# Performance work log

Hardware: AMD Instinct MI355X
Metric: run time of the kernel (lower is better)

The kernel has to match this reference:

```python
import jax, jax.numpy as jnp
import numpy as np

B, L, E, H = 1, 4096, 1024, 16
D = E // H
EPS = 1e-6


def setup_inputs() -> dict:
    key = jax.random.key(0)
    k1, k2, k3 = jax.random.split(key, 3)
    # fan-in scaled init to keep activations sane
    x = jax.random.normal(k1, (B, L, E), dtype=jnp.float32)
    qkv_w = jax.random.normal(k2, (E, 3 * E), dtype=jnp.float32) / np.sqrt(E)
    qkv_b = jnp.zeros((3 * E,), dtype=jnp.float32)
    out_w = jax.random.normal(k3, (E, E), dtype=jnp.float32) / np.sqrt(E)
    out_b = jnp.zeros((E,), dtype=jnp.float32)
    return {"x": x, "qkv_w": qkv_w, "qkv_b": qkv_b, "out_w": out_w, "out_b": out_b}


def reference(x, qkv_w, qkv_b, out_w, out_b):
    b, l, e = x.shape
    qkv = x @ qkv_w + qkv_b                      # (B, L, 3E)
    q, k, v = jnp.split(qkv, 3, axis=-1)
    # (B, L, E) -> (B, H, L, D)
    q = q.reshape(b, l, H, D).transpose(0, 2, 1, 3)
    k = k.reshape(b, l, H, D).transpose(0, 2, 1, 3)
    v = v.reshape(b, l, H, D).transpose(0, 2, 1, 3)
    q_prime = jax.nn.elu(q) + 1.0
    k_prime = jax.nn.elu(k) + 1.0
    # cumulative sum of per-position outer products k'_l v_l^T : (B,H,L,D,D)
    kv_prod = jnp.einsum('bhld,bhle->bhlde', k_prime, v)
    kv_cumsum = jnp.cumsum(kv_prod, axis=2)
    context = jnp.einsum('bhld,bhlde->bhle', q_prime, kv_cumsum)  # (B,H,L,D)
    k_cumsum = jnp.cumsum(k_prime, axis=2)                        # (B,H,L,D)
    norm = jnp.einsum('bhld,bhld->bhl', q_prime, k_cumsum)        # (B,H,L)
    output = context / (norm[..., None] + EPS)
    output = output.transpose(0, 2, 1, 3).reshape(b, l, e)
    return output @ out_w + out_b
```

## Files before the change

kernel.cpp:

```cpp
#include <hip/hip_runtime.h>
#include <cstddef>
#include <cstdint>

#define L_SEQ 4096
#define EMB   1024
#define NH    16
#define HD    64
#define N3    3072
#define CHUNK 64
#define NCHUNK 64
#define EPS 1e-6f

typedef __attribute__((ext_vector_type(8))) short   bf16x8;
typedef __attribute__((ext_vector_type(4))) short   bf16x4;
typedef __attribute__((ext_vector_type(4))) float   floatx4;

#define AS1 __attribute__((address_space(1)))
#define AS3 __attribute__((address_space(3)))

__device__ __forceinline__ void gload_lds16(const void* g, void* l) {
    __builtin_amdgcn_global_load_lds((AS1 const unsigned int*)g,
                                     (AS3 unsigned int*)l, 16, 0, 0);
}

__device__ __forceinline__ short f2bf(float f) {
    union { float f; unsigned u; } a; a.f = f;
    unsigned r = a.u + 0x7fffu + ((a.u >> 16) & 1u);
    return (short)(r >> 16);
}
__device__ __forceinline__ float bf2f(short s) {
    union { unsigned u; float f; } a; a.u = ((unsigned)(unsigned short)s) << 16;
    return a.f;
}

__global__ __launch_bounds__(256)
void convert_bf16(const float* __restrict__ in, short* __restrict__ out, int n8)
{
    const int i = blockIdx.x * 256 + threadIdx.x;
    if (i < n8) {
        const floatx4 a = *(const floatx4*)(in + (size_t)i * 8);
        const floatx4 b = *(const floatx4*)(in + (size_t)i * 8 + 4);
        bf16x8 o;
        o[0] = f2bf(a[0]); o[1] = f2bf(a[1]); o[2] = f2bf(a[2]); o[3] = f2bf(a[3]);
        o[4] = f2bf(b[0]); o[5] = f2bf(b[1]); o[6] = f2bf(b[2]); o[7] = f2bf(b[3]);
        *(bf16x8*)(out + (size_t)i * 8) = o;
    }
}

__global__ __launch_bounds__(256)
void transpose_bf16(const float* __restrict__ W, short* __restrict__ WT,
                    int K, int N)
{
    __shared__ float t[64][65];
    const int bx = blockIdx.x, by = blockIdx.y;
    const int tid = threadIdx.x;
    const int r  = tid >> 4;
    const int c4 = (tid & 15) << 2;
#pragma unroll
    for (int s = 0; s < 4; ++s) {
        const int k = r + s * 16;
        const floatx4 v = *(const floatx4*)&W[(size_t)(by * 64 + k) * N + bx * 64 + c4];
        t[k][c4 + 0] = v[0]; t[k][c4 + 1] = v[1];
        t[k][c4 + 2] = v[2]; t[k][c4 + 3] = v[3];
    }
    __syncthreads();
#pragma unroll
    for (int s = 0; s < 4; ++s) {
        const int n = r + s * 16;
        bf16x4 o;
        o[0] = f2bf(t[c4 + 0][n]); o[1] = f2bf(t[c4 + 1][n]);
        o[2] = f2bf(t[c4 + 2][n]); o[3] = f2bf(t[c4 + 3][n]);
        *(bf16x4*)&WT[(size_t)(bx * 64 + n) * K + by * 64 + c4] = o;
    }
}

template<int MODE>
__global__ __launch_bounds__(256)
void mfma_gemm(const short* __restrict__ A, const short* __restrict__ BT,
               const float* __restrict__ bias,
               short* __restrict__ OQ, short* __restrict__ OK, short* __restrict__ OV,
               float* __restrict__ OF, int N, int K)
{
    __shared__ short Asm[128 * 32];
    __shared__ short Bsm[128 * 32];
    const int tid  = threadIdx.x;
    const int lane = tid & 63;
    const int wave = tid >> 6;
    const int wm = (wave >> 1) * 64;
    const int wn = (wave & 1) * 64;
    const int bx = blockIdx.x;
    const int by = blockIdx.y;
    const int frow = lane & 15;
    const int fko  = (lane >> 4) << 3;

    const short* Ab = A  + (size_t)(by * 128) * K;
    const short* Bb = BT + (size_t)(bx * 128) * K;

    floatx4 acc[4][4] = {};

    for (int k0 = 0; k0 < K; k0 += 32) {
#pragma unroll
        for (int q = 0; q < 2; ++q) {
            const int ia = q * 256 + tid;
            const int row = ia >> 2;
            const int kc  = (ia & 3) << 3;
            gload_lds16(Ab + (size_t)row * K + k0 + kc, &Asm[ia << 3]);
            gload_lds16(Bb + (size_t)row * K + k0 + kc, &Bsm[ia << 3]);
        }
        __syncthreads();
        bf16x8 af[4], bfv[4];
#pragma unroll
        for (int mi = 0; mi < 4; ++mi)
            af[mi] = *(const bf16x8*)&Asm[(wm + mi * 16 + frow) * 32 + fko];
#pragma unroll
        for (int ni = 0; ni < 4; ++ni)
            bfv[ni] = *(const bf16x8*)&Bsm[(wn + ni * 16 + frow) * 32 + fko];
#pragma unroll
        for (int mi = 0; mi < 4; ++mi)
#pragma unroll
            for (int ni = 0; ni < 4; ++ni)
                acc[mi][ni] = __builtin_amdgcn_mfma_f32_16x16x32_bf16(
                    af[mi], bfv[ni], acc[mi][ni], 0, 0, 0);
        __syncthreads();
    }

    const int rq = (lane >> 4) << 2;
#pragma unroll
    for (int ni = 0; ni < 4; ++ni) {
        const int n = bx * 128 + wn + ni * 16 + frow;
        const float bv = bias[n];
        if (MODE == 0) {
            const int rsel = n >> 10;
            const int nn = n & 1023;
            const int h  = nn >> 6;
            const int d  = nn & 63;
            short* base = (rsel == 0) ? OQ : (rsel == 1 ? OK : OV);
            const bool do_elu = (rsel < 2);
#pragma unroll
            for (int mi = 0; mi < 4; ++mi) {
#pragma unroll
                for (int r = 0; r < 4; ++r) {
                    const int m = by * 128 + wm + mi * 16 + rq + r;
                    float v = acc[mi][ni][r] + bv;
                    if (do_elu) v = (v > 0.f) ? (v + 1.f) : expf(v);
                    base[((size_t)(h * L_SEQ + m)) * HD + d] = f2bf(v);
                }
            }
        } else {
#pragma unroll
            for (int mi = 0; mi < 4; ++mi) {
#pragma unroll
                for (int r = 0; r < 4; ++r) {
                    const int m = by * 128 + wm + mi * 16 + rq + r;
                    OF[(size_t)m * N + n] = acc[mi][ni][r] + bv;
                }
            }
        }
    }
}

__global__ __launch_bounds__(256)
void chunk_state(const short* __restrict__ Kb, const short* __restrict__ Vb,
                 float* __restrict__ ScT, float* __restrict__ zc)
{
    __shared__ float Kc[CHUNK * HD];
    __shared__ float Vc[CHUNK * HD];
    const int c = blockIdx.x, h = blockIdx.y;
    const int tid = threadIdx.x;
    const short* Kg = Kb + ((size_t)h * L_SEQ + (size_t)c * CHUNK) * HD;
    const short* Vg = Vb + ((size_t)h * L_SEQ + (size_t)c * CHUNK) * HD;
#pragma unroll
    for (int q = 0; q < 2; ++q) {
        const int idx = q * 256 + tid;
        const bf16x8 kv = *(const bf16x8*)&Kg[idx * 8];
        const bf16x8 vv = *(const bf16x8*)&Vg[idx * 8];
#pragma unroll
        for (int j = 0; j < 8; ++j) {
            Kc[idx * 8 + j] = bf2f(kv[j]);
            Vc[idx * 8 + j] = bf2f(vv[j]);
        }
    }
    __syncthreads();
    const int e0 = (tid >> 4) << 2;
    const int d0 = (tid & 15) << 2;
    float acc[4][4] = {{0.f}};
    for (int l = 0; l < CHUNK; ++l) {
        const floatx4 ve = *(const floatx4*)&Vc[l * HD + e0];
        const floatx4 kd = *(const floatx4*)&Kc[l * HD + d0];
#pragma unroll
        for (int a = 0; a < 4; ++a)
#pragma unroll
            for (int b = 0; b < 4; ++b)
                acc[a][b] += ve[a] * kd[b];
    }
    float* Sout = ScT + ((size_t)(h * NCHUNK + c)) * HD * HD;
#pragma unroll
    for (int a = 0; a < 4; ++a) {
        floatx4 o; o[0] = acc[a][0]; o[1] = acc[a][1]; o[2] = acc[a][2]; o[3] = acc[a][3];
        *(floatx4*)&Sout[(e0 + a) * HD + d0] = o;
    }
    if (tid < HD) {
        float z = 0.f;
        for (int l = 0; l < CHUNK; ++l) z += Kc[l * HD + tid];
        zc[((size_t)(h * NCHUNK + c)) * HD + tid] = z;
    }
}

__global__ __launch_bounds__(256)
void prefix_scan(const float* __restrict__ ScT, const float* __restrict__ zc,
                 short* __restrict__ S0b)
{
    const int g = blockIdx.x * 256 + threadIdx.x;
    const int h  = g >> 12;
    const int ed = g & 4095;
    const int e  = ed >> 6;
    const int d  = ed & 63;
    float run = 0.f;
    for (int c = 0; c < NCHUNK; ++c) {
        S0b[((size_t)(h * NCHUNK + c) * 65 + e) * 64 + d] = f2bf(run);
        run += ScT[((size_t)(h * NCHUNK + c)) * 4096 + ed];
    }
    if (g < NH * HD) {
        const int h2 = g >> 6, d2 = g & 63;
        float rz = 0.f;
        for (int c = 0; c < NCHUNK; ++c) {
            S0b[((size_t)(h2 * NCHUNK + c) * 65 + 64) * 64 + d2] = f2bf(rz);
            rz += zc[((size_t)(h2 * NCHUNK + c)) * HD + d2];
        }
    }
}

#define SP 72

__global__ __launch_bounds__(256)
void chunk_attn(const short* __restrict__ Qb, const short* __restrict__ Kb,
                const short* __restrict__ Vb, const short* __restrict__ S0b,
                short* __restrict__ attn)
{
    __shared__ __align__(16) short Qs[64 * SP];
    __shared__ __align__(16) short Ks[64 * SP];
    __shared__ __align__(16) short As[64 * SP];
    __shared__ __align__(16) short Vs[80 * SP];
    __shared__ __align__(16) short Ss[80 * SP];
    const int c = blockIdx.x, h = blockIdx.y;
    const int tid = threadIdx.x, lane = tid & 63, wave = tid >> 6;
    const size_t rb = ((size_t)h * L_SEQ + (size_t)c * CHUNK) * HD;
    const short* Qg = Qb + rb;
    const short* Kg = Kb + rb;
    const short* Vg = Vb + rb;
    const short* Sg = S0b + (size_t)(h * NCHUNK + c) * 65 * 64;

#pragma unroll
    for (int q = 0; q < 2; ++q) {
        const int idx = q * 256 + tid;
        const int row = idx >> 3, c8 = (idx & 7) << 3;
        *(bf16x8*)&Qs[row * SP + c8] = *(const bf16x8*)&Qg[row * 64 + c8];
        *(bf16x8*)&Ks[row * SP + c8] = *(const bf16x8*)&Kg[row * 64 + c8];
        const bf16x8 vv = *(const bf16x8*)&Vg[row * 64 + c8];
#pragma unroll
        for (int j = 0; j < 8; ++j) Vs[(c8 + j) * SP + row] = vv[j];
    }
    if (tid < 64) Vs[64 * SP + tid] = (short)0x3F80;
    for (int idx = tid; idx < 520; idx += 256) {
        const int row = idx >> 3, c8 = (idx & 7) << 3;
        *(bf16x8*)&Ss[row * SP + c8] = *(const bf16x8*)&Sg[row * 64 + c8];
    }
    __syncthreads();

    const int frow = lane & 15;
    const int quad = lane >> 4;
    const int fko  = quad << 3;
    const int wm   = wave << 4;

    const bf16x8 qf0 = *(const bf16x8*)&Qs[(wm + frow) * SP + fko];
    const bf16x8 qf1 = *(const bf16x8*)&Qs[(wm + frow) * SP + 32 + fko];

    floatx4 sacc[4] = {};
#pragma unroll
    for (int n = 0; n < 4; ++n) {
        const bf16x8 kf0 = *(const bf16x8*)&Ks[(n * 16 + frow) * SP + fko];
        const bf16x8 kf1 = *(const bf16x8*)&Ks[(n * 16 + frow) * SP + 32 + fko];
        sacc[n] = __builtin_amdgcn_mfma_f32_16x16x32_bf16(qf0, kf0, sacc[n], 0, 0, 0);
        sacc[n] = __builtin_amdgcn_mfma_f32_16x16x32_bf16(qf1, kf1, sacc[n], 0, 0, 0);
    }
#pragma unroll
    for (int n = 0; n < 4; ++n)
#pragma unroll
        for (int r = 0; r < 4; ++r) {
            const int i = wm + quad * 4 + r;
            const int j = n * 16 + frow;
            As[i * SP + j] = (j <= i) ? f2bf(sacc[n][r]) : (short)0;
        }
    __syncthreads();

    const bf16x8 af0 = *(const bf16x8*)&As[(wm + frow) * SP + fko];
    const bf16x8 af1 = *(const bf16x8*)&As[(wm + frow) * SP + 32 + fko];
    floatx4 oacc[5] = {};
#pragma unroll
    for (int n = 0; n < 5; ++n) {
        const bf16x8 vf0 = *(const bf16x8*)&Vs[(n * 16 + frow) * SP + fko];
        const bf16x8 vf1 = *(const bf16x8*)&Vs[(n * 16 + frow) * SP + 32 + fko];
        oacc[n] = __builtin_amdgcn_mfma_f32_16x16x32_bf16(af0, vf0, oacc[n], 0, 0, 0);
        oacc[n] = __builtin_amdgcn_mfma_f32_16x16x32_bf16(af1, vf1, oacc[n], 0, 0, 0);
        const bf16x8 sf0 = *(const bf16x8*)&Ss[(n * 16 + frow) * SP + fko];
        const bf16x8 sf1 = *(const bf16x8*)&Ss[(n * 16 + frow) * SP + 32 + fko];
        oacc[n] = __builtin_amdgcn_mfma_f32_16x16x32_bf16(qf0, sf0, oacc[n], 0, 0, 0);
        oacc[n] = __builtin_amdgcn_mfma_f32_16x16x32_bf16(qf1, sf1, oacc[n], 0, 0, 0);
    }

#pragma unroll
    for (int r = 0; r < 4; ++r) {
        const float norm = __shfl(oacc[4][r], lane & 48) + EPS;
        const float inv = 1.f / norm;
        const int i = wm + quad * 4 + r;
        short* dst = attn + (size_t)(c * CHUNK + i) * EMB + h * HD;
#pragma unroll
        for (int n = 0; n < 4; ++n)
            dst[n * 16 + frow] = f2bf(oacc[n][r] * inv);
    }
}

extern "C" void kernel_launch(void* const* d_in, const int* in_sizes, int n_in,
                              void* d_out, int out_size, void* d_ws, size_t ws_size,
                              hipStream_t stream)
{
    const float* x     = (const float*)d_in[0];
    const float* qkv_w = (const float*)d_in[1];
    const float* qkv_b = (const float*)d_in[2];
    const float* out_w = (const float*)d_in[3];
    const float* out_b = (const float*)d_in[4];
    float* out = (float*)d_out;

    short* ws    = (short*)d_ws;
    short* Qb    = ws;
    short* Kb    = Qb + 4194304;
    short* Vb    = Kb + 4194304;
    short* xb    = Vb + 4194304;
    short* qwt   = xb + 4194304;
    short* owt   = qwt + 3145728;
    short* attnb = owt + 1048576;
    short* S0b   = attnb + 4194304;
    float* ScT   = (float*)(S0b + 4259840);
    float* zc    = ScT + 4194304;

    convert_bf16<<<dim3(2048), 256, 0, stream>>>(x, xb, 524288);
    transpose_bf16<<<dim3(N3 / 64, EMB / 64), 256, 0, stream>>>(qkv_w, qwt, EMB, N3);
    transpose_bf16<<<dim3(EMB / 64, EMB / 64), 256, 0, stream>>>(out_w, owt, EMB, EMB);
    mfma_gemm<0><<<dim3(N3 / 128, L_SEQ / 128), 256, 0, stream>>>(
        xb, qwt, qkv_b, Qb, Kb, Vb, nullptr, N3, EMB);
    chunk_state<<<dim3(NCHUNK, NH), 256, 0, stream>>>(Kb, Vb, ScT, zc);
    prefix_scan<<<dim3((NH * 4096) / 256), 256, 0, stream>>>(ScT, zc, S0b);
    chunk_attn<<<dim3(NCHUNK, NH), 256, 0, stream>>>(Qb, Kb, Vb, S0b, attnb);
    mfma_gemm<1><<<dim3(EMB / 128, L_SEQ / 128), 256, 0, stream>>>(
        attnb, owt, out_b, nullptr, nullptr, nullptr, out, EMB, EMB);
}
```

Baseline: 187.7 us.

## Merge prep kernels, stage GEMM and attention epilogues through LDS, bf16 chunk states

The three preprocessing kernels (x conversion and the two weight transposes) become one launch. The QKV GEMM and chunk_attn epilogues now stage results in shared memory so each thread writes 16-byte vectors instead of scattered 2-byte stores. Per-chunk states are stored in bf16 rather than fp32, halving that traffic, and the prefix scan batches its loads eight at a time. The costs are a larger shared-memory allocation in the GEMM, which may lower occupancy, and some precision loss from rounding the intermediate states to bf16.

```diff
diff --git a/kernel.cpp b/kernel.cpp
--- a/kernel.cpp
+++ b/kernel.cpp
@@ -33,27 +33,11 @@
     return a.f;
 }
 
-__global__ __launch_bounds__(256)
-void convert_bf16(const float* __restrict__ in, short* __restrict__ out, int n8)
-{
-    const int i = blockIdx.x * 256 + threadIdx.x;
-    if (i < n8) {
-        const floatx4 a = *(const floatx4*)(in + (size_t)i * 8);
-        const floatx4 b = *(const floatx4*)(in + (size_t)i * 8 + 4);
-        bf16x8 o;
-        o[0] = f2bf(a[0]); o[1] = f2bf(a[1]); o[2] = f2bf(a[2]); o[3] = f2bf(a[3]);
-        o[4] = f2bf(b[0]); o[5] = f2bf(b[1]); o[6] = f2bf(b[2]); o[7] = f2bf(b[3]);
-        *(bf16x8*)(out + (size_t)i * 8) = o;
-    }
-}
-
-__global__ __launch_bounds__(256)
-void transpose_bf16(const float* __restrict__ W, short* __restrict__ WT,
-                    int K, int N)
-{
-    __shared__ float t[64][65];
-    const int bx = blockIdx.x, by = blockIdx.y;
-    const int tid = threadIdx.x;
+__device__ __forceinline__ void transpose_tile(const float* __restrict__ W,
+                                               short* __restrict__ WT,
+                                               int K, int N, int bx, int by,
+                                               float (*t)[65], int tid)
+{
     const int r  = tid >> 4;
     const int c4 = (tid & 15) << 2;
 #pragma unroll
@@ -74,6 +58,33 @@
     }
 }
 
+__global__ __launch_bounds__(256)
+void prep(const float* __restrict__ x, short* __restrict__ xb,
+          const float* __restrict__ qkv_w, short* __restrict__ qwt,
+          const float* __restrict__ out_w, short* __restrict__ owt)
+{
+    __shared__ float t[64][65];
+    const int b = blockIdx.x;
+    const int tid = threadIdx.x;
+    if (b < 2048) {
+        const int i = b * 256 + tid;
+        const floatx4 a = *(const floatx4*)(x + (size_t)i * 8);
+        const floatx4 c = *(const floatx4*)(x + (size_t)i * 8 + 4);
+        bf16x8 o;
+        o[0] = f2bf(a[0]); o[1] = f2bf(a[1]); o[2] = f2bf(a[2]); o[3] = f2bf(a[3]);
+        o[4] = f2bf(c[0]); o[5] = f2bf(c[1]); o[6] = f2bf(c[2]); o[7] = f2bf(c[3]);
+        *(bf16x8*)(xb + (size_t)i * 8) = o;
+    } else if (b < 2048 + 768) {
+        const int u = b - 2048;
+        transpose_tile(qkv_w, qwt, EMB, N3, u % 48, u / 48, t, tid);
+    } else {
+        const int u = b - 2816;
+        transpose_tile(out_w, owt, EMB, EMB, u & 15, u >> 4, t, tid);
+    }
+}
+
+#define CST 136
+
 template<int MODE>
 __global__ __launch_bounds__(256)
 void mfma_gemm(const short* __restrict__ A, const short* __restrict__ BT,
@@ -81,8 +92,9 @@
                short* __restrict__ OQ, short* __restrict__ OK, short* __restrict__ OV,
                float* __restrict__ OF, int N, int K)
 {
-    __shared__ short Asm[128 * 32];
-    __shared__ short Bsm[128 * 32];
+    __shared__ __align__(16) short smem[128 * CST];
+    short* Asm = smem;
+    short* Bsm = smem + 4096;
     const int tid  = threadIdx.x;
     const int lane = tid & 63;
     const int wave = tid >> 6;
@@ -125,43 +137,54 @@
     }
 
     const int rq = (lane >> 4) << 2;
-#pragma unroll
-    for (int ni = 0; ni < 4; ++ni) {
-        const int n = bx * 128 + wn + ni * 16 + frow;
-        const float bv = bias[n];
-        if (MODE == 0) {
-            const int rsel = n >> 10;
-            const int nn = n & 1023;
-            const int h  = nn >> 6;
-            const int d  = nn & 63;
+    if (MODE == 0) {
+#pragma unroll
+        for (int ni = 0; ni < 4; ++ni) {
+            const int n = bx * 128 + wn + ni * 16 + frow;
+            const float bv = bias[n];
+            const bool do_elu = (n >> 10) < 2;
+#pragma unroll
+            for (int mi = 0; mi < 4; ++mi)
+#pragma unroll
+                for (int r = 0; r < 4; ++r) {
+                    float v = acc[mi][ni][r] + bv;
+                    if (do_elu) v = (v > 0.f) ? (v + 1.f) : __expf(v);
+                    smem[(wm + mi * 16 + rq + r) * CST + wn + ni * 16 + frow] = f2bf(v);
+                }
+        }
+        __syncthreads();
+#pragma unroll
+        for (int t = 0; t < 8; ++t) {
+            const int idx = t * 256 + tid;
+            const int mm = idx >> 4;
+            const int c8 = (idx & 15) << 3;
+            const bf16x8 val = *(const bf16x8*)&smem[mm * CST + c8];
+            const int n0 = bx * 128 + c8;
+            const int rsel = n0 >> 10;
+            const int h  = (n0 & 1023) >> 6;
+            const int d  = n0 & 63;
             short* base = (rsel == 0) ? OQ : (rsel == 1 ? OK : OV);
-            const bool do_elu = (rsel < 2);
-#pragma unroll
-            for (int mi = 0; mi < 4; ++mi) {
-#pragma unroll
-                for (int r = 0; r < 4; ++r) {
-                    const int m = by * 128 + wm + mi * 16 + rq + r;
-                    float v = acc[mi][ni][r] + bv;
-                    if (do_elu) v = (v > 0.f) ? (v + 1.f) : expf(v);
-                    base[((size_t)(h * L_SEQ + m)) * HD + d] = f2bf(v);
-                }
-            }
-        } else {
-#pragma unroll
-            for (int mi = 0; mi < 4; ++mi) {
+            *(bf16x8*)&base[((size_t)(h * L_SEQ + by * 128 + mm)) * HD + d] = val;
+        }
+    } else {
+#pragma unroll
+        for (int ni = 0; ni < 4; ++ni) {
+            const int n = bx * 128 + wn + ni * 16 + frow;
+            const float bv = bias[n];
+#pragma unroll
+            for (int mi = 0; mi < 4; ++mi)
 #pragma unroll
                 for (int r = 0; r < 4; ++r) {
                     const int m = by * 128 + wm + mi * 16 + rq + r;
                     OF[(size_t)m * N + n] = acc[mi][ni][r] + bv;
                 }
-            }
         }
     }
 }
 
 __global__ __launch_bounds__(256)
 void chunk_state(const short* __restrict__ Kb, const short* __restrict__ Vb,
-                 float* __restrict__ ScT, float* __restrict__ zc)
+                 short* __restrict__ ScTb, float* __restrict__ zc)
 {
     __shared__ float Kc[CHUNK * HD];
     __shared__ float Vc[CHUNK * HD];
@@ -193,11 +216,13 @@
             for (int b = 0; b < 4; ++b)
                 acc[a][b] += ve[a] * kd[b];
     }
-    float* Sout = ScT + ((size_t)(h * NCHUNK + c)) * HD * HD;
+    short* Sout = ScTb + (size_t)(h * NCHUNK + c) * 4096;
 #pragma unroll
     for (int a = 0; a < 4; ++a) {
-        floatx4 o; o[0] = acc[a][0]; o[1] = acc[a][1]; o[2] = acc[a][2]; o[3] = acc[a][3];
-        *(floatx4*)&Sout[(e0 + a) * HD + d0] = o;
+        bf16x4 o;
+        o[0] = f2bf(acc[a][0]); o[1] = f2bf(acc[a][1]);
+        o[2] = f2bf(acc[a][2]); o[3] = f2bf(acc[a][3]);
+        *(bf16x4*)&Sout[(e0 + a) * HD + d0] = o;
     }
     if (tid < HD) {
         float z = 0.f;
@@ -207,7 +232,7 @@
 }
 
 __global__ __launch_bounds__(256)
-void prefix_scan(const float* __restrict__ ScT, const float* __restrict__ zc,
+void prefix_scan(const short* __restrict__ ScTb, const float* __restrict__ zc,
                  short* __restrict__ S0b)
 {
     const int g = blockIdx.x * 256 + threadIdx.x;
@@ -215,17 +240,31 @@
     const int ed = g & 4095;
     const int e  = ed >> 6;
     const int d  = ed & 63;
+    const short* src = ScTb + (size_t)h * NCHUNK * 4096 + ed;
     float run = 0.f;
-    for (int c = 0; c < NCHUNK; ++c) {
-        S0b[((size_t)(h * NCHUNK + c) * 65 + e) * 64 + d] = f2bf(run);
-        run += ScT[((size_t)(h * NCHUNK + c)) * 4096 + ed];
+    for (int cb = 0; cb < NCHUNK; cb += 8) {
+        short v[8];
+#pragma unroll
+        for (int u = 0; u < 8; ++u) v[u] = src[(size_t)(cb + u) * 4096];
+#pragma unroll
+        for (int u = 0; u < 8; ++u) {
+            S0b[((size_t)((h * NCHUNK + cb + u) * 65 + e)) * 64 + d] = f2bf(run);
+            run += bf2f(v[u]);
+        }
     }
     if (g < NH * HD) {
         const int h2 = g >> 6, d2 = g & 63;
         float rz = 0.f;
-        for (int c = 0; c < NCHUNK; ++c) {
-            S0b[((size_t)(h2 * NCHUNK + c) * 65 + 64) * 64 + d2] = f2bf(rz);
-            rz += zc[((size_t)(h2 * NCHUNK + c)) * HD + d2];
+        for (int cb = 0; cb < NCHUNK; cb += 8) {
+            float w[8];
+#pragma unroll
+            for (int u = 0; u < 8; ++u)
+                w[u] = zc[((size_t)(h2 * NCHUNK + cb + u)) * HD + d2];
+#pragma unroll
+            for (int u = 0; u < 8; ++u) {
+                S0b[((size_t)((h2 * NCHUNK + cb + u) * 65 + 64)) * 64 + d2] = f2bf(rz);
+                rz += w[u];
+            }
         }
     }
 }
@@ -313,10 +352,17 @@
         const float norm = __shfl(oacc[4][r], lane & 48) + EPS;
         const float inv = 1.f / norm;
         const int i = wm + quad * 4 + r;
-        short* dst = attn + (size_t)(c * CHUNK + i) * EMB + h * HD;
 #pragma unroll
         for (int n = 0; n < 4; ++n)
-            dst[n * 16 + frow] = f2bf(oacc[n][r] * inv);
+            As[i * SP + n * 16 + frow] = f2bf(oacc[n][r] * inv);
+    }
+    __syncthreads();
+#pragma unroll
+    for (int t = 0; t < 2; ++t) {
+        const int idx = t * 256 + tid;
+        const int row = idx >> 3, c8 = (idx & 7) << 3;
+        *(bf16x8*)&attn[(size_t)(c * CHUNK + row) * EMB + h * HD + c8] =
+            *(const bf16x8*)&As[row * SP + c8];
     }
 }
 
@@ -340,16 +386,14 @@
     short* owt   = qwt + 3145728;
     short* attnb = owt + 1048576;
     short* S0b   = attnb + 4194304;
-    float* ScT   = (float*)(S0b + 4259840);
-    float* zc    = ScT + 4194304;
-
-    convert_bf16<<<dim3(2048), 256, 0, stream>>>(x, xb, 524288);
-    transpose_bf16<<<dim3(N3 / 64, EMB / 64), 256, 0, stream>>>(qkv_w, qwt, EMB, N3);
-    transpose_bf16<<<dim3(EMB / 64, EMB / 64), 256, 0, stream>>>(out_w, owt, EMB, EMB);
+    short* ScTb  = S0b + 4259840;
+    float* zc    = (float*)(ScTb + 4194304);
+
+    prep<<<dim3(3072), 256, 0, stream>>>(x, xb, qkv_w, qwt, out_w, owt);
     mfma_gemm<0><<<dim3(N3 / 128, L_SEQ / 128), 256, 0, stream>>>(
         xb, qwt, qkv_b, Qb, Kb, Vb, nullptr, N3, EMB);
-    chunk_state<<<dim3(NCHUNK, NH), 256, 0, stream>>>(Kb, Vb, ScT, zc);
-    prefix_scan<<<dim3((NH * 4096) / 256), 256, 0, stream>>>(ScT, zc, S0b);
+    chunk_state<<<dim3(NCHUNK, NH), 256, 0, stream>>>(Kb, Vb, ScTb, zc);
+    prefix_scan<<<dim3((NH * 4096) / 256), 256, 0, stream>>>(ScTb, zc, S0b);
     chunk_attn<<<dim3(NCHUNK, NH), 256, 0, stream>>>(Qb, Kb, Vb, S0b, attnb);
     mfma_gemm<1><<<dim3(EMB / 128, L_SEQ / 128), 256, 0, stream>>>(
         attnb, owt, out_b, nullptr, nullptr, nullptr, out, EMB, EMB);
```

Result: faster. 179.9 us (-4.2%).
